# Kernel optimization log

Measured on AMD Instinct MI355X. Metric: run time of the kernel, lower is better.

## Reference

```python
import jax, jax.numpy as jnp
import numpy as np

NH = 256   # nh_rnn
V = 21     # joints
TC = 60    # cont time dim
CC = 4     # cont channels
DCT_N = 60
T_HIS = 30
HORIZON = 60
BS = 256


def _lin(x, w, b):
    # torch nn.Linear convention: w is [out, in]
    return x @ w.T + b


def setup_inputs() -> dict:
    key = jax.random.key(0)
    ks = iter(jax.random.split(key, 48))

    def rn(shape, s=1.0):
        return jax.random.normal(next(ks), shape, dtype=jnp.float32) * jnp.float32(s)

    inp = {}
    inp["x"] = rn((T_HIS, BS, 63))
    inp["cont"] = rn((BS, TC, V * CC))
    inp["cont_mask"] = jnp.ones((BS, TC), jnp.float32)  # never used (per docstring)
    inp["dct_m"] = rn((DCT_N, T_HIS + HORIZON), 0.1)
    inp["idct_m"] = rn((T_HIS + HORIZON, DCT_N), 0.1)
    inp["root_idx"] = jnp.array([42, 43, 44], dtype=jnp.int32)
    inp["horizon"] = HORIZON

    # --- STSGCN_layer(cont): learned temporal/spatial adjacencies + 1x1 convs + BN(folded) + PReLU ---
    inp["T_c"] = rn((V, TC, TC), 1.0 / np.sqrt(TC))
    inp["A_c"] = rn((TC, V, V), 1.0 / np.sqrt(V))
    inp["conv_w"] = rn((NH, CC), 0.5)
    inp["conv_b"] = rn((NH,), 0.1)
    inp["bn1_scale"] = 1.0 + rn((NH,), 0.1)
    inp["bn1_shift"] = rn((NH,), 0.1)
    inp["resconv_w"] = rn((NH, CC), 0.5)
    inp["resconv_b"] = rn((NH,), 0.1)
    inp["bnr_scale"] = 1.0 + rn((NH,), 0.1)
    inp["bnr_shift"] = rn((NH,), 0.1)
    inp["prelu_a"] = jnp.float32(0.25)

    # tiny MLP encoders
    inp["te1_w"] = rn((10, TC), 1.0 / np.sqrt(TC)); inp["te1_b"] = rn((10,), 0.1)
    inp["te2_w"] = rn((1, 10), 1.0 / np.sqrt(10)); inp["te2_b"] = rn((1,), 0.1)
    inp["ne1_w"] = rn((10, V), 1.0 / np.sqrt(V)); inp["ne1_b"] = rn((10,), 0.1)
    inp["ne2_w"] = rn((1, 10), 1.0 / np.sqrt(10)); inp["ne2_b"] = rn((1,), 0.1)

    # residual MLP head
    din = DCT_N * 3 + NH
    inp["g1_w"] = rn((NH, din), 1.0 / np.sqrt(din)); inp["g1_b"] = rn((NH,), 0.1)
    inp["g2a_w"] = rn((NH, NH), 1.0 / np.sqrt(NH)); inp["g2a_b"] = rn((NH,), 0.1)
    inp["g2b_w"] = rn((NH, NH), 1.0 / np.sqrt(NH)); inp["g2b_b"] = rn((NH,), 0.1)
    inp["g3a_w"] = rn((NH, NH), 1.0 / np.sqrt(NH)); inp["g3a_b"] = rn((NH,), 0.1)
    inp["g3b_w"] = rn((NH, NH), 1.0 / np.sqrt(NH)); inp["g3b_b"] = rn((NH,), 0.1)
    inp["g4_w"] = rn((DCT_N * 3, NH), 1.0 / np.sqrt(NH)); inp["g4_b"] = rn((DCT_N * 3,), 0.1)
    return inp


def reference(x, cont, cont_mask, dct_m, idct_m, root_idx, horizon,
              T_c, A_c, conv_w, conv_b, bn1_scale, bn1_shift,
              resconv_w, resconv_b, bnr_scale, bnr_shift, prelu_a,
              te1_w, te1_b, te2_w, te2_b, ne1_w, ne1_b, ne2_w, ne2_b,
              g1_w, g1_b, g2a_w, g2a_b, g2b_w, g2b_b,
              g3a_w, g3a_b, g3b_w, g3b_b, g4_w, g4_b):
    t_his, bs, _ = x.shape

    # --- root history padded with last frame, then batched DCT ---
    pad_idx = jnp.concatenate([jnp.arange(t_his), jnp.full((horizon,), t_his - 1)])
    root_his = x[:, :, root_idx][pad_idx].transpose(1, 0, 2)                 # [bs, 90, 3]
    root_his_dct = jnp.einsum('dt,btk->bdk', dct_m, root_his).reshape(bs, -1)  # [bs, 180]

    # --- STSGCN layer on contact stream: [b, 4, 60, 21] ---
    xc = cont.reshape(bs, TC, V, CC).transpose(0, 3, 1, 2)                   # [b,c,t,v]
    res = jnp.einsum('nctv,oc->notv', xc, resconv_w) + resconv_b[None, :, None, None]
    res = res * bnr_scale[None, :, None, None] + bnr_shift[None, :, None, None]
    g = jnp.einsum('nctv,vtq->ncqv', xc, T_c)    # temporal adjacency
    g = jnp.einsum('nctv,tvw->nctw', g, A_c)     # spatial adjacency
    h = jnp.einsum('nctv,oc->notv', g, conv_w) + conv_b[None, :, None, None]
    h = h * bn1_scale[None, :, None, None] + bn1_shift[None, :, None, None]
    h = h + res
    h = jnp.where(h >= 0, h, prelu_a * h)        # PReLU, [b, 256, 60, 21]

    # --- time encoder: collapse t=60 -> 1 ---
    ht = h.transpose(0, 1, 3, 2).reshape(bs, NH * V, TC)
    ht = jnp.tanh(_lin(jnp.tanh(_lin(ht, te1_w, te1_b)), te2_w, te2_b))[..., 0]
    # --- node encoder: collapse v=21 -> 1 ---
    hn = ht.reshape(bs, NH, V)
    hcont = jnp.tanh(_lin(jnp.tanh(_lin(hn, ne1_w, ne1_b)), ne2_w, ne2_b))[..., 0]  # [bs, 256]

    # --- residual MLP head on DCT coefficients ---
    rh = jnp.tanh(_lin(jnp.concatenate([root_his_dct, hcont], axis=1), g1_w, g1_b))
    rh = jnp.tanh(_lin(jnp.tanh(_lin(rh, g2a_w, g2a_b)), g2b_w, g2b_b)) + rh
    rh = jnp.tanh(_lin(jnp.tanh(_lin(rh, g3a_w, g3a_b)), g3b_w, g3b_b)) + rh
    root_pred = _lin(rh, g4_w, g4_b) + root_his_dct                          # [bs, 180]
    root_traj = jnp.einsum('td,bdk->btk', idct_m, root_pred.reshape(bs, DCT_N, 3))
    return root_traj                                                          # [bs, 90, 3]
```

## Files before the change

### kernel.cpp

```cpp
#include <hip/hip_runtime.h>

#define NHID 256
#define NV   21
#define NT   60
#define NC   4
#define NDCT 60
#define THIS 30
#define NBS  256
#define WSROW 448

typedef float f32x2 __attribute__((ext_vector_type(2)));
typedef float f32x4 __attribute__((ext_vector_type(4)));

__device__ __forceinline__ float ftanh(float x) {
    float e = __expf(2.0f * x);
    return 1.0f - __fdividef(2.0f, e + 1.0f);
}

__global__ __launch_bounds__(1024, 4) void k_p1(
    const float* __restrict__ x,
    const float* __restrict__ cont,
    const float* __restrict__ dct_m,
    const int* __restrict__ root_idx,
    const float* __restrict__ T_c, const float* __restrict__ A_c,
    const float* __restrict__ conv_w, const float* __restrict__ conv_b,
    const float* __restrict__ bn1_scale, const float* __restrict__ bn1_shift,
    const float* __restrict__ resconv_w, const float* __restrict__ resconv_b,
    const float* __restrict__ bnr_scale, const float* __restrict__ bnr_shift,
    const float* __restrict__ prelu_a_p,
    const float* __restrict__ te1_w, const float* __restrict__ te1_b,
    const float* __restrict__ te2_w, const float* __restrict__ te2_b,
    const float* __restrict__ ne1_w, const float* __restrict__ ne1_b,
    const float* __restrict__ ne2_w, const float* __restrict__ ne2_b,
    float* __restrict__ ws)
{
    __shared__ __align__(16) float xc_lds[5040];
    __shared__ __align__(16) float g_lds[5040];
    __shared__ __align__(16) float g2_lds[5040];

    const int n   = blockIdx.x;
    const int tid = threadIdx.x;

    {
        const float4* src = (const float4*)(cont + n * 5040);
        float4* dst = (float4*)xc_lds;
        for (int i = tid; i < 1260; i += 1024) dst[i] = src[i];
    }
    __syncthreads();

    for (int task = tid; task < 630; task += 1024) {
        int v  = task / 30;
        int q0 = (task - v * 30) * 2;
        const float* tc = T_c + v * 3600 + q0;
        f32x4 a0 = {0.f,0.f,0.f,0.f}, a1 = {0.f,0.f,0.f,0.f};
        #pragma unroll 4
        for (int t = 0; t < 60; ++t) {
            f32x4 xcv = *(const f32x4*)(xc_lds + t * 84 + v * 4);
            float2 tq = *(const float2*)(tc + t * 60);
            a0 += xcv * tq.x;
            a1 += xcv * tq.y;
        }
        *(f32x4*)(g_lds + q0 * 84 + v * 4)       = a0;
        *(f32x4*)(g_lds + (q0 + 1) * 84 + v * 4) = a1;
    }
    __syncthreads();

    for (int task = tid; task < 660; task += 1024) {
        int t  = task / 11;
        int w0 = (task - t * 11) * 2;
        const bool has2 = (w0 < 20);
        const float* ac = A_c + t * 441 + w0;
        f32x4 a0 = {0.f,0.f,0.f,0.f}, a1 = {0.f,0.f,0.f,0.f};
        #pragma unroll
        for (int v = 0; v < 21; ++v) {
            f32x4 gv = *(const f32x4*)(g_lds + t * 84 + v * 4);
            float b0 = ac[v * 21];
            float b1 = has2 ? ac[v * 21 + 1] : 0.f;
            a0 += gv * b0;
            a1 += gv * b1;
        }
        *(f32x4*)(g2_lds + t * 84 + w0 * 4) = a0;
        if (has2) *(f32x4*)(g2_lds + t * 84 + (w0 + 1) * 4) = a1;
    }
    __syncthreads();

    float* tew = g_lds;

    if (tid < 720) {
        int t = tid / 12, j = tid - t * 12;
        tew[tid] = (j < 10) ? te1_w[j * 60 + t] : 0.f;
    } else if (tid >= 720 && tid < 900) {
        int r = tid - 720;
        int d = r / 3, k = r - d * 3;
        int ri = root_idx[k];
        const float* xp = x + n * 63 + ri;
        const float* dm = dct_m + d * 90;
        float acc = 0.f;
        #pragma unroll
        for (int t = 0; t < 30; ++t)
            acc += dm[t] * xp[t * 16128];
        float wl = 0.f;
        #pragma unroll
        for (int t = 30; t < 90; ++t)
            wl += dm[t];
        acc += wl * xp[29 * 16128];
        ws[n * WSROW + r] = acc;
    }
    __syncthreads();

    {
        const int og = tid >> 3;
        const int part = tid & 7;
        const int vstart = (part < 5) ? part * 3 : 15 + (part - 5) * 2;
        const int vcount = (part < 5) ? 3 : 2;

        const float pa = prelu_a_p[0];

        f32x2 cA01[2], cA23[2], cB01[2], cB23[2];
        float cC[2];
        #pragma unroll
        for (int g = 0; g < 2; ++g) {
            int o = og * 2 + g;
            float s1 = bn1_scale[o], sr = bnr_scale[o];
            cA01[g] = (f32x2){conv_w[o*4+0] * s1, conv_w[o*4+1] * s1};
            cA23[g] = (f32x2){conv_w[o*4+2] * s1, conv_w[o*4+3] * s1};
            cB01[g] = (f32x2){resconv_w[o*4+0] * sr, resconv_w[o*4+1] * sr};
            cB23[g] = (f32x2){resconv_w[o*4+2] * sr, resconv_w[o*4+3] * sr};
            cC[g] = conv_b[o] * s1 + bn1_shift[o] + resconv_b[o] * sr + bnr_shift[o];
        }

        float tw2[10], tb1[10];
        #pragma unroll
        for (int j = 0; j < 10; ++j) { tw2[j] = te2_w[j]; tb1[j] = te1_b[j]; }
        const float tb2 = te2_b[0];

        float wacc[2][10];
        #pragma unroll
        for (int g = 0; g < 2; ++g)
            #pragma unroll
            for (int j = 0; j < 10; ++j) wacc[g][j] = 0.f;

        for (int vi = 0; vi < vcount; ++vi) {
            int v = vstart + vi;
            f32x2 u2[2][5];
            #pragma unroll
            for (int g = 0; g < 2; ++g)
                #pragma unroll
                for (int p = 0; p < 5; ++p)
                    u2[g][p] = (f32x2){tb1[2*p], tb1[2*p+1]};

            const float* xcp = xc_lds + v * 4;
            const float* g2p = g2_lds + v * 4;
            for (int t = 0; t < 60; ++t) {
                f32x4 xcv = *(const f32x4*)(xcp + t * 84);
                f32x4 g2v = *(const f32x4*)(g2p + t * 84);
                const float* twp = tew + t * 12;
                f32x4 t03 = *(const f32x4*)(twp);
                f32x4 t47 = *(const f32x4*)(twp + 4);
                f32x2 t89 = *(const f32x2*)(twp + 8);
                f32x2 tw[5] = { {t03.x,t03.y}, {t03.z,t03.w},
                                {t47.x,t47.y}, {t47.z,t47.w}, t89 };
                f32x2 g01 = {g2v.x, g2v.y}, g23 = {g2v.z, g2v.w};
                f32x2 x01 = {xcv.x, xcv.y}, x23 = {xcv.z, xcv.w};
                #pragma unroll
                for (int g = 0; g < 2; ++g) {
                    f32x2 hv = {cC[g], 0.f};
                    hv += cA01[g] * g01;
                    hv += cA23[g] * g23;
                    hv += cB01[g] * x01;
                    hv += cB23[g] * x23;
                    float h = hv.x + hv.y;
                    h = fmaxf(h, 0.f) + pa * fminf(h, 0.f);
                    #pragma unroll
                    for (int p = 0; p < 5; ++p)
                        u2[g][p] += h * tw[p];
                }
            }

            float nw[10];
            #pragma unroll
            for (int j = 0; j < 10; ++j) nw[j] = ne1_w[j * 21 + v];
            #pragma unroll
            for (int g = 0; g < 2; ++g) {
                float s = tb2;
                #pragma unroll
                for (int p = 0; p < 5; ++p) {
                    s += ftanh(u2[g][p].x) * tw2[2*p];
                    s += ftanh(u2[g][p].y) * tw2[2*p+1];
                }
                s = ftanh(s);
                #pragma unroll
                for (int j = 0; j < 10; ++j) wacc[g][j] += s * nw[j];
            }
        }

        #pragma unroll
        for (int d = 1; d < 8; d <<= 1)
            #pragma unroll
            for (int g = 0; g < 2; ++g)
                #pragma unroll
                for (int j = 0; j < 10; ++j)
                    wacc[g][j] += __shfl_xor(wacc[g][j], d, 64);

        if (part == 0) {
            float nw2[10];
            #pragma unroll
            for (int j = 0; j < 10; ++j) nw2[j] = ne2_w[j];
            float nb2 = ne2_b[0];
            #pragma unroll
            for (int g = 0; g < 2; ++g) {
                int o = og * 2 + g;
                float s = nb2;
                #pragma unroll
                for (int j = 0; j < 10; ++j)
                    s += ftanh(wacc[g][j] + ne1_b[j]) * nw2[j];
                ws[n * WSROW + 180 + o] = ftanh(s);
            }
        }
    }
}

__global__ __launch_bounds__(1024, 4) void k_p2(
    const float* __restrict__ ws,
    const float* __restrict__ g1_w, const float* __restrict__ g1_b,
    const float* __restrict__ g2a_w, const float* __restrict__ g2a_b,
    const float* __restrict__ g2b_w, const float* __restrict__ g2b_b,
    const float* __restrict__ g3a_w, const float* __restrict__ g3a_b,
    const float* __restrict__ g3b_w, const float* __restrict__ g3b_b,
    const float* __restrict__ g4_w, const float* __restrict__ g4_b,
    const float* __restrict__ idct_m, float* __restrict__ out)
{
    __shared__ __align__(16) float in2[436];
    __shared__ __align__(16) float aL[256];
    __shared__ __align__(16) float bL[256];
    __shared__ __align__(16) float rp[180];

    const int n   = blockIdx.x;
    const int tid = threadIdx.x;

    if (tid < 109) {
        *(f32x4*)(in2 + tid * 4) = *(const f32x4*)(ws + n * WSROW + tid * 4);
    }
    __syncthreads();

    const int gid = tid >> 2;
    const int sub = tid & 3;

#define DENSE(KDIM, NCHUNK, W, SRC, BODY)                                      \
    {                                                                          \
        f32x4 accA = {0.f,0.f,0.f,0.f}, accB = {0.f,0.f,0.f,0.f};              \
        _Pragma("unroll")                                                      \
        for (int s = 0; s < (NCHUNK + 7) / 8; ++s) {                           \
            int c4 = s * 8 + sub;                                              \
            if (c4 < NCHUNK) {                                                 \
                f32x4 av = *(const f32x4*)&SRC[c4 * 4];                        \
                f32x4 wv = *(const f32x4*)&W[gid * KDIM + c4 * 4];             \
                accA += av * wv;                                               \
            }                                                                  \
            int c4b = s * 8 + 4 + sub;                                         \
            if (c4b < NCHUNK) {                                                \
                f32x4 av = *(const f32x4*)&SRC[c4b * 4];                       \
                f32x4 wv = *(const f32x4*)&W[gid * KDIM + c4b * 4];            \
                accB += av * wv;                                               \
            }                                                                  \
        }                                                                      \
        f32x4 accv = accA + accB;                                              \
        float acc = (accv.x + accv.y) + (accv.z + accv.w);                     \
        acc += __shfl_xor(acc, 1, 64);                                         \
        acc += __shfl_xor(acc, 2, 64);                                         \
        if (sub == 0) { int o = gid; float sumv = acc; BODY }                  \
    }                                                                          \
    __syncthreads();

    DENSE(436, 109, g1_w, in2, { aL[o] = ftanh(sumv + g1_b[o]); })
    DENSE(256, 64, g2a_w, aL, { bL[o] = ftanh(sumv + g2a_b[o]); })
    DENSE(256, 64, g2b_w, bL, { aL[o] = ftanh(sumv + g2b_b[o]) + aL[o]; })
    DENSE(256, 64, g3a_w, aL, { bL[o] = ftanh(sumv + g3a_b[o]); })
    DENSE(256, 64, g3b_w, bL, { aL[o] = ftanh(sumv + g3b_b[o]) + aL[o]; })
    DENSE(256, 64, g4_w, aL, { if (o < 180) rp[o] = sumv + g4_b[o] + in2[o]; })

    if (tid < 270) {
        int t = tid / 3;
        int k = tid - t * 3;
        const float* im = idct_m + t * 60;
        const float* rpp = rp + k;
        float acc = 0.f;
        #pragma unroll
        for (int d = 0; d < 60; ++d)
            acc += im[d] * rpp[d * 3];
        out[n * 270 + tid] = acc;
    }
}

extern "C" void kernel_launch(void* const* d_in, const int* in_sizes, int n_in,
                              void* d_out, int out_size, void* d_ws, size_t ws_size,
                              hipStream_t stream)
{
    const float* x        = (const float*)d_in[0];
    const float* cont     = (const float*)d_in[1];
    const float* dct_m    = (const float*)d_in[3];
    const float* idct_m   = (const float*)d_in[4];
    const int*   root_idx = (const int*)d_in[5];
    const float* T_c      = (const float*)d_in[7];
    const float* A_c      = (const float*)d_in[8];
    const float* conv_w   = (const float*)d_in[9];
    const float* conv_b   = (const float*)d_in[10];
    const float* bn1_s    = (const float*)d_in[11];
    const float* bn1_sh   = (const float*)d_in[12];
    const float* rconv_w  = (const float*)d_in[13];
    const float* rconv_b  = (const float*)d_in[14];
    const float* bnr_s    = (const float*)d_in[15];
    const float* bnr_sh   = (const float*)d_in[16];
    const float* prelu_a  = (const float*)d_in[17];
    const float* te1_w    = (const float*)d_in[18];
    const float* te1_b    = (const float*)d_in[19];
    const float* te2_w    = (const float*)d_in[20];
    const float* te2_b    = (const float*)d_in[21];
    const float* ne1_w    = (const float*)d_in[22];
    const float* ne1_b    = (const float*)d_in[23];
    const float* ne2_w    = (const float*)d_in[24];
    const float* ne2_b    = (const float*)d_in[25];
    const float* g1_w     = (const float*)d_in[26];
    const float* g1_b     = (const float*)d_in[27];
    const float* g2a_w    = (const float*)d_in[28];
    const float* g2a_b    = (const float*)d_in[29];
    const float* g2b_w    = (const float*)d_in[30];
    const float* g2b_b    = (const float*)d_in[31];
    const float* g3a_w    = (const float*)d_in[32];
    const float* g3a_b    = (const float*)d_in[33];
    const float* g3b_w    = (const float*)d_in[34];
    const float* g3b_b    = (const float*)d_in[35];
    const float* g4_w     = (const float*)d_in[36];
    const float* g4_b     = (const float*)d_in[37];

    float* wsf = (float*)d_ws;

    k_p1<<<NBS, 1024, 0, stream>>>(x, cont, dct_m, root_idx,
                                   T_c, A_c,
                                   conv_w, conv_b, bn1_s, bn1_sh,
                                   rconv_w, rconv_b, bnr_s, bnr_sh,
                                   prelu_a,
                                   te1_w, te1_b, te2_w, te2_b,
                                   ne1_w, ne1_b, ne2_w, ne2_b,
                                   wsf);

    k_p2<<<NBS, 1024, 0, stream>>>(wsf,
                                   g1_w, g1_b, g2a_w, g2a_b, g2b_w, g2b_b,
                                   g3a_w, g3a_b, g3b_w, g3b_b, g4_w, g4_b,
                                   idct_m, (float*)d_out);
}
```

Measured before the change: 248.0 us.

## Halve k_p1 block size with 4 channels per thread; batch two samples per k_p2 block

k_p1 now runs with 512 threads per block, and each thread computes 4 output channels instead of 2. This lets the per-thread LDS reads of xc, g2 and the time-encoder weights be reused across more channels, at the cost of more registers and less parallelism in the earlier phases. k_p2 processes two batch samples per block, so each dense-layer weight vector loaded from global memory is applied to both samples. This halves weight traffic and the number of blocks, with 128 blocks left on the GPU.

Measured after the change: 239.6 us. 1.04x faster.

```diff
diff --git a/kernel.cpp b/kernel.cpp
--- a/kernel.cpp
+++ b/kernel.cpp
@@ -17,7 +17,7 @@
     return 1.0f - __fdividef(2.0f, e + 1.0f);
 }
 
-__global__ __launch_bounds__(1024, 4) void k_p1(
+__global__ __launch_bounds__(512, 2) void k_p1(
     const float* __restrict__ x,
     const float* __restrict__ cont,
     const float* __restrict__ dct_m,
@@ -44,11 +44,11 @@
     {
         const float4* src = (const float4*)(cont + n * 5040);
         float4* dst = (float4*)xc_lds;
-        for (int i = tid; i < 1260; i += 1024) dst[i] = src[i];
-    }
-    __syncthreads();
-
-    for (int task = tid; task < 630; task += 1024) {
+        for (int i = tid; i < 1260; i += 512) dst[i] = src[i];
+    }
+    __syncthreads();
+
+    for (int task = tid; task < 630; task += 512) {
         int v  = task / 30;
         int q0 = (task - v * 30) * 2;
         const float* tc = T_c + v * 3600 + q0;
@@ -65,7 +65,7 @@
     }
     __syncthreads();
 
-    for (int task = tid; task < 660; task += 1024) {
+    for (int task = tid; task < 660; task += 512) {
         int t  = task / 11;
         int w0 = (task - t * 11) * 2;
         const bool has2 = (w0 < 20);
@@ -86,12 +86,12 @@
 
     float* tew = g_lds;
 
-    if (tid < 720) {
-        int t = tid / 12, j = tid - t * 12;
-        tew[tid] = (j < 10) ? te1_w[j * 60 + t] : 0.f;
-    } else if (tid >= 720 && tid < 900) {
-        int r = tid - 720;
-        int d = r / 3, k = r - d * 3;
+    for (int i = tid; i < 720; i += 512) {
+        int t = i / 12, j = i - t * 12;
+        tew[i] = (j < 10) ? te1_w[j * 60 + t] : 0.f;
+    }
+    if (tid < 180) {
+        int d = tid / 3, k = tid - d * 3;
         int ri = root_idx[k];
         const float* xp = x + n * 63 + ri;
         const float* dm = dct_m + d * 90;
@@ -104,7 +104,7 @@
         for (int t = 30; t < 90; ++t)
             wl += dm[t];
         acc += wl * xp[29 * 16128];
-        ws[n * WSROW + r] = acc;
+        ws[n * WSROW + tid] = acc;
     }
     __syncthreads();
 
@@ -113,14 +113,15 @@
         const int part = tid & 7;
         const int vstart = (part < 5) ? part * 3 : 15 + (part - 5) * 2;
         const int vcount = (part < 5) ? 3 : 2;
+        const int obase = og * 4;
 
         const float pa = prelu_a_p[0];
 
-        f32x2 cA01[2], cA23[2], cB01[2], cB23[2];
-        float cC[2];
-        #pragma unroll
-        for (int g = 0; g < 2; ++g) {
-            int o = og * 2 + g;
+        f32x2 cA01[4], cA23[4], cB01[4], cB23[4];
+        float cC[4];
+        #pragma unroll
+        for (int g = 0; g < 4; ++g) {
+            int o = obase + g;
             float s1 = bn1_scale[o], sr = bnr_scale[o];
             cA01[g] = (f32x2){conv_w[o*4+0] * s1, conv_w[o*4+1] * s1};
             cA23[g] = (f32x2){conv_w[o*4+2] * s1, conv_w[o*4+3] * s1};
@@ -134,17 +135,17 @@
         for (int j = 0; j < 10; ++j) { tw2[j] = te2_w[j]; tb1[j] = te1_b[j]; }
         const float tb2 = te2_b[0];
 
-        float wacc[2][10];
-        #pragma unroll
-        for (int g = 0; g < 2; ++g)
+        float wacc[4][10];
+        #pragma unroll
+        for (int g = 0; g < 4; ++g)
             #pragma unroll
             for (int j = 0; j < 10; ++j) wacc[g][j] = 0.f;
 
         for (int vi = 0; vi < vcount; ++vi) {
             int v = vstart + vi;
-            f32x2 u2[2][5];
-            #pragma unroll
-            for (int g = 0; g < 2; ++g)
+            f32x2 u2[4][5];
+            #pragma unroll
+            for (int g = 0; g < 4; ++g)
                 #pragma unroll
                 for (int p = 0; p < 5; ++p)
                     u2[g][p] = (f32x2){tb1[2*p], tb1[2*p+1]};
@@ -163,7 +164,7 @@
                 f32x2 g01 = {g2v.x, g2v.y}, g23 = {g2v.z, g2v.w};
                 f32x2 x01 = {xcv.x, xcv.y}, x23 = {xcv.z, xcv.w};
                 #pragma unroll
-                for (int g = 0; g < 2; ++g) {
+                for (int g = 0; g < 4; ++g) {
                     f32x2 hv = {cC[g], 0.f};
                     hv += cA01[g] * g01;
                     hv += cA23[g] * g23;
@@ -181,7 +182,7 @@
             #pragma unroll
             for (int j = 0; j < 10; ++j) nw[j] = ne1_w[j * 21 + v];
             #pragma unroll
-            for (int g = 0; g < 2; ++g) {
+            for (int g = 0; g < 4; ++g) {
                 float s = tb2;
                 #pragma unroll
                 for (int p = 0; p < 5; ++p) {
@@ -197,7 +198,7 @@
         #pragma unroll
         for (int d = 1; d < 8; d <<= 1)
             #pragma unroll
-            for (int g = 0; g < 2; ++g)
+            for (int g = 0; g < 4; ++g)
                 #pragma unroll
                 for (int j = 0; j < 10; ++j)
                     wacc[g][j] += __shfl_xor(wacc[g][j], d, 64);
@@ -208,8 +209,8 @@
             for (int j = 0; j < 10; ++j) nw2[j] = ne2_w[j];
             float nb2 = ne2_b[0];
             #pragma unroll
-            for (int g = 0; g < 2; ++g) {
-                int o = og * 2 + g;
+            for (int g = 0; g < 4; ++g) {
+                int o = obase + g;
                 float s = nb2;
                 #pragma unroll
                 for (int j = 0; j < 10; ++j)
@@ -230,65 +231,73 @@
     const float* __restrict__ g4_w, const float* __restrict__ g4_b,
     const float* __restrict__ idct_m, float* __restrict__ out)
 {
-    __shared__ __align__(16) float in2[436];
-    __shared__ __align__(16) float aL[256];
-    __shared__ __align__(16) float bL[256];
-    __shared__ __align__(16) float rp[180];
-
-    const int n   = blockIdx.x;
+    __shared__ __align__(16) float in2[2][436];
+    __shared__ __align__(16) float aL[2][256];
+    __shared__ __align__(16) float bL[2][256];
+    __shared__ __align__(16) float rp[2][180];
+
+    const int n0  = blockIdx.x * 2;
     const int tid = threadIdx.x;
 
-    if (tid < 109) {
-        *(f32x4*)(in2 + tid * 4) = *(const f32x4*)(ws + n * WSROW + tid * 4);
+    if (tid < 218) {
+        int bn = tid / 109, i = tid - bn * 109;
+        *(f32x4*)(&in2[bn][i * 4]) = *(const f32x4*)(ws + (n0 + bn) * WSROW + i * 4);
     }
     __syncthreads();
 
     const int gid = tid >> 2;
     const int sub = tid & 3;
 
-#define DENSE(KDIM, NCHUNK, W, SRC, BODY)                                      \
+#define DENSE(KDIM, NCHUNK, W, S0, S1, BODY)                                   \
     {                                                                          \
-        f32x4 accA = {0.f,0.f,0.f,0.f}, accB = {0.f,0.f,0.f,0.f};              \
+        f32x4 acc0 = {0.f,0.f,0.f,0.f}, acc1 = {0.f,0.f,0.f,0.f};              \
         _Pragma("unroll")                                                      \
-        for (int s = 0; s < (NCHUNK + 7) / 8; ++s) {                           \
-            int c4 = s * 8 + sub;                                              \
+        for (int s = 0; s < (NCHUNK + 3) / 4; ++s) {                           \
+            int c4 = s * 4 + sub;                                              \
             if (c4 < NCHUNK) {                                                 \
-                f32x4 av = *(const f32x4*)&SRC[c4 * 4];                        \
                 f32x4 wv = *(const f32x4*)&W[gid * KDIM + c4 * 4];             \
-                accA += av * wv;                                               \
-            }                                                                  \
-            int c4b = s * 8 + 4 + sub;                                         \
-            if (c4b < NCHUNK) {                                                \
-                f32x4 av = *(const f32x4*)&SRC[c4b * 4];                       \
-                f32x4 wv = *(const f32x4*)&W[gid * KDIM + c4b * 4];            \
-                accB += av * wv;                                               \
+                f32x4 a0 = *(const f32x4*)&S0[c4 * 4];                         \
+                f32x4 a1 = *(const f32x4*)&S1[c4 * 4];                         \
+                acc0 += a0 * wv;                                               \
+                acc1 += a1 * wv;                                               \
             }                                                                  \
         }                                                                      \
-        f32x4 accv = accA + accB;                                              \
-        float acc = (accv.x + accv.y) + (accv.z + accv.w);                     \
-        acc += __shfl_xor(acc, 1, 64);                                         \
-        acc += __shfl_xor(acc, 2, 64);                                         \
-        if (sub == 0) { int o = gid; float sumv = acc; BODY }                  \
+        float r0 = (acc0.x + acc0.y) + (acc0.z + acc0.w);                      \
+        float r1 = (acc1.x + acc1.y) + (acc1.z + acc1.w);                      \
+        r0 += __shfl_xor(r0, 1, 64);  r1 += __shfl_xor(r1, 1, 64);             \
+        r0 += __shfl_xor(r0, 2, 64);  r1 += __shfl_xor(r1, 2, 64);             \
+        if (sub == 0) { int o = gid; BODY }                                    \
     }                                                                          \
     __syncthreads();
 
-    DENSE(436, 109, g1_w, in2, { aL[o] = ftanh(sumv + g1_b[o]); })
-    DENSE(256, 64, g2a_w, aL, { bL[o] = ftanh(sumv + g2a_b[o]); })
-    DENSE(256, 64, g2b_w, bL, { aL[o] = ftanh(sumv + g2b_b[o]) + aL[o]; })
-    DENSE(256, 64, g3a_w, aL, { bL[o] = ftanh(sumv + g3a_b[o]); })
-    DENSE(256, 64, g3b_w, bL, { aL[o] = ftanh(sumv + g3b_b[o]) + aL[o]; })
-    DENSE(256, 64, g4_w, aL, { if (o < 180) rp[o] = sumv + g4_b[o] + in2[o]; })
-
-    if (tid < 270) {
-        int t = tid / 3;
-        int k = tid - t * 3;
+    DENSE(436, 109, g1_w, in2[0], in2[1],
+        { aL[0][o] = ftanh(r0 + g1_b[o]); aL[1][o] = ftanh(r1 + g1_b[o]); })
+    DENSE(256, 64, g2a_w, aL[0], aL[1],
+        { bL[0][o] = ftanh(r0 + g2a_b[o]); bL[1][o] = ftanh(r1 + g2a_b[o]); })
+    DENSE(256, 64, g2b_w, bL[0], bL[1],
+        { aL[0][o] = ftanh(r0 + g2b_b[o]) + aL[0][o];
+          aL[1][o] = ftanh(r1 + g2b_b[o]) + aL[1][o]; })
+    DENSE(256, 64, g3a_w, aL[0], aL[1],
+        { bL[0][o] = ftanh(r0 + g3a_b[o]); bL[1][o] = ftanh(r1 + g3a_b[o]); })
+    DENSE(256, 64, g3b_w, bL[0], bL[1],
+        { aL[0][o] = ftanh(r0 + g3b_b[o]) + aL[0][o];
+          aL[1][o] = ftanh(r1 + g3b_b[o]) + aL[1][o]; })
+    DENSE(256, 64, g4_w, aL[0], aL[1],
+        { if (o < 180) { rp[0][o] = r0 + g4_b[o] + in2[0][o];
+                         rp[1][o] = r1 + g4_b[o] + in2[1][o]; } })
+
+    for (int idx = tid; idx < 2 * 270; idx += 1024) {
+        int bn = idx / 270;
+        int r = idx - bn * 270;
+        int t = r / 3;
+        int k = r - t * 3;
         const float* im = idct_m + t * 60;
-        const float* rpp = rp + k;
+        const float* rpp = &rp[bn][k];
         float acc = 0.f;
         #pragma unroll
         for (int d = 0; d < 60; ++d)
             acc += im[d] * rpp[d * 3];
-        out[n * 270 + tid] = acc;
+        out[(n0 + bn) * 270 + r] = acc;
     }
 }
 
@@ -335,17 +344,17 @@
 
     float* wsf = (float*)d_ws;
 
-    k_p1<<<NBS, 1024, 0, stream>>>(x, cont, dct_m, root_idx,
-                                   T_c, A_c,
-                                   conv_w, conv_b, bn1_s, bn1_sh,
-                                   rconv_w, rconv_b, bnr_s, bnr_sh,
-                                   prelu_a,
-                                   te1_w, te1_b, te2_w, te2_b,
-                                   ne1_w, ne1_b, ne2_w, ne2_b,
-                                   wsf);
-
-    k_p2<<<NBS, 1024, 0, stream>>>(wsf,
-                                   g1_w, g1_b, g2a_w, g2a_b, g2b_w, g2b_b,
-                                   g3a_w, g3a_b, g3b_w, g3b_b, g4_w, g4_b,
-                                   idct_m, (float*)d_out);
+    k_p1<<<NBS, 512, 0, stream>>>(x, cont, dct_m, root_idx,
+                                  T_c, A_c,
+                                  conv_w, conv_b, bn1_s, bn1_sh,
+                                  rconv_w, rconv_b, bnr_s, bnr_sh,
+                                  prelu_a,
+                                  te1_w, te1_b, te2_w, te2_b,
+                                  ne1_w, ne1_b, ne2_w, ne2_b,
+                                  wsf);
+
+    k_p2<<<NBS / 2, 1024, 0, stream>>>(wsf,
+                                       g1_w, g1_b, g2a_w, g2a_b, g2b_w, g2b_b,
+                                       g3a_w, g3a_b, g3b_w, g3b_b, g4_w, g4_b,
+                                       idct_m, (float*)d_out);
 }
```
